# Optimization experiments

Measured on AMD Instinct MI355X. Metric: run time of the kernel, lower is better.

## Reference

```python
import jax, jax.numpy as jnp
import numpy as np

NEG_INF = -1e12  # stanza's constant.INFINITY_NUMBER


def setup_inputs() -> dict:
    key = jax.random.key(0)
    k1, k2, k3, k4, k5, k6 = jax.random.split(key, 6)
    B, S, D = 128, 8192, 128
    inp = jax.random.normal(k1, (B, D), dtype=jnp.float32)
    context = jax.random.normal(k2, (B, S, D), dtype=jnp.float32)
    mask = jax.random.bernoulli(k3, 0.3, (B, S))  # True = masked out
    # learned params (torch nn.Linear convention: y = x @ W.T)
    W = jax.random.normal(k4, (D, D), dtype=jnp.float32) / np.sqrt(D)
    V = jax.random.normal(k5, (1, D), dtype=jnp.float32) / np.sqrt(D)
    Wout = jax.random.normal(k6, (D, 2 * D), dtype=jnp.float32) / np.sqrt(2 * D)
    return {"input": inp, "context": context, "mask": mask, "W": W, "V": V, "Wout": Wout}


def reference(input, context, mask, W, V, Wout):
    # u = ReLU(W x): per-batch, identical across source positions -> compute once
    u = jax.nn.relu(jnp.einsum('bd,ed->be', input, W))          # [B, D]
    v = jax.nn.relu(jnp.einsum('bsd,ed->bse', context, W))      # [B, S, D]
    # a = V . (u o v)
    attn = jnp.einsum('be,bse,e->bs', u, v, V[0])               # [B, S]
    attn = jnp.where(mask, NEG_INF, attn)
    attn = jax.nn.softmax(attn, axis=1)
    weighted = jnp.einsum('bs,bsd->bd', attn, context)          # [B, D]
    h_tilde = jnp.tanh(jnp.einsum('bf,ef->be', jnp.concatenate([weighted, input], axis=1), Wout))
    return (h_tilde, attn)
```

## Files before the change

kernel.cpp:

```cpp
#include <hip/hip_runtime.h>


#define BB 128
#define SS 8192
#define DD 128

typedef float f32x4_t __attribute__((ext_vector_type(4)));
typedef short bf16x8_t __attribute__((ext_vector_type(8)));
typedef unsigned short u16x8_t __attribute__((ext_vector_type(8)));
typedef unsigned int u32x4_t __attribute__((ext_vector_type(4)));
typedef int i32x4_t __attribute__((ext_vector_type(4)));

__device__ __forceinline__ unsigned short f2bf(float x) {
  unsigned u = __builtin_bit_cast(unsigned, x);
  unsigned r = (u + 0x7FFFu + ((u >> 16) & 1u)) >> 16;
  return (unsigned short)r;
}
__device__ __forceinline__ float bf2f(unsigned short h) {
  unsigned u = ((unsigned)h) << 16;
  return __builtin_bit_cast(float, u);
}
__device__ __forceinline__ unsigned cvtpk(float a, float b) {
  unsigned r;
  asm("v_cvt_pk_bf16_f32 %0, %1, %2" : "=v"(r) : "v"(a), "v"(b));
  return r;
}

__global__ void k_detect(const unsigned int* __restrict__ mw, unsigned int* __restrict__ flag) {
  int i = blockIdx.x * 256 + threadIdx.x;
  unsigned v = mw[i];
  unsigned f = 0;
  if (v == 0x3F800000u) f = 2u;
  else if (v > 1u) f = 1u;
  if (f) atomicOr(flag, f);
}

__global__ void k_prep(const float* __restrict__ inp, const float* __restrict__ Wg,
                       const float* __restrict__ Vg, unsigned short* __restrict__ Whi,
                       unsigned short* __restrict__ Wlo, float* __restrict__ wv) {
  const int b = blockIdx.x, tid = threadIdx.x;
  {
    int i = b * DD + tid;
    float x = Wg[i];
    unsigned short h = f2bf(x);
    Whi[i] = h;
    Wlo[i] = f2bf(x - bf2f(h));
  }
  __shared__ float xin[DD];
  xin[tid] = inp[b * DD + tid];
  __syncthreads();
  const float* wr = Wg + tid * DD;
  float s = 0.f;
#pragma unroll 8
  for (int d = 0; d < DD; ++d) s += xin[d] * wr[d];
  wv[b * DD + tid] = fmaxf(s, 0.f) * Vg[tid];
}

__launch_bounds__(512, 1)
__global__ void k_logits(const float* __restrict__ ctx, const unsigned short* __restrict__ Whi,
                         const unsigned short* __restrict__ Wlo, const float* __restrict__ wv,
                         const void* __restrict__ maskp, const unsigned int* __restrict__ flag,
                         float* __restrict__ logits, float* __restrict__ Wslice,
                         float* __restrict__ stats) {
  __shared__ unsigned short WPKH[16384];
  __shared__ unsigned short WPKL[16384];
  __shared__ float wl[DD];
  __shared__ float WB[8][DD];
  __shared__ float MS[8][2];

  const int tid = threadIdx.x;
  const int b = blockIdx.y;
  const int slice = blockIdx.x;
  const int wave = tid >> 6;
  const int lane = tid & 63;
  const int lr = lane & 15;
  const int lg = lane >> 4;
  const unsigned mode = *flag;

  const long rowb0 = (long)b * SS + (long)slice * 2048 + (long)wave * 256;

  f32x4_t xA[8], xB[8];
  auto issue = [&](f32x4_t (&x)[8], long grow, int rt) {
    const float* rp = ctx + (grow + rt * 16 + lr) * (long)DD + lg * 8;
#pragma unroll
    for (int ks = 0; ks < 4; ++ks) {
      x[ks * 2]     = *(const f32x4_t*)(rp + ks * 32);
      x[ks * 2 + 1] = *(const f32x4_t*)(rp + ks * 32 + 4);
    }
  };

  issue(xA, rowb0, 0);

#pragma unroll
  for (int jj = 0; jj < 4; ++jj) {
    int p = tid + jj * 512;
    int frag = p >> 6;
    int li = p & 63;
    int et = frag >> 2, ks = frag & 3;
    int lg2 = li >> 4, lr2 = li & 15;
    int src = (et * 16 + lr2) * DD + ks * 32 + lg2 * 8;
    *(u16x8_t*)(&WPKH[p * 8]) = *(const u16x8_t*)(&Whi[src]);
    *(u16x8_t*)(&WPKL[p * 8]) = *(const u16x8_t*)(&Wlo[src]);
  }
  if (tid < DD) wl[tid] = wv[b * DD + tid];
  __syncthreads();

  float wfreg[8];
#pragma unroll
  for (int et = 0; et < 8; ++et) wfreg[et] = wl[et * 16 + lr];

  float m_run = -3.4e38f, s_run = 0.f;
  f32x4_t wacc[8];
#pragma unroll
  for (int k = 0; k < 8; ++k) wacc[k] = f32x4_t{0.f, 0.f, 0.f, 0.f};

  auto process = [&](const f32x4_t (&x)[8], long grow, int rt) {
    bf16x8_t a[4];
#pragma unroll
    for (int ks = 0; ks < 4; ++ks) {
      u32x4_t hh;
      hh[0] = cvtpk(x[ks * 2][0], x[ks * 2][1]);
      hh[1] = cvtpk(x[ks * 2][2], x[ks * 2][3]);
      hh[2] = cvtpk(x[ks * 2 + 1][0], x[ks * 2 + 1][1]);
      hh[3] = cvtpk(x[ks * 2 + 1][2], x[ks * 2 + 1][3]);
      a[ks] = __builtin_bit_cast(bf16x8_t, hh);
    }
    f32x4_t part = {0.f, 0.f, 0.f, 0.f};
#pragma unroll
    for (int et = 0; et < 8; ++et) {
      f32x4_t v1 = {0.f, 0.f, 0.f, 0.f};
      f32x4_t v2 = v1;
#pragma unroll
      for (int ks = 0; ks < 4; ++ks) {
        const int pidx = ((((et << 2) | ks) << 6) | lane) << 3;
        bf16x8_t bh = *(const bf16x8_t*)(&WPKH[pidx]);
        bf16x8_t bl = *(const bf16x8_t*)(&WPKL[pidx]);
        v1 = __builtin_amdgcn_mfma_f32_16x16x32_bf16(a[ks], bh, v1, 0, 0, 0);
        v2 = __builtin_amdgcn_mfma_f32_16x16x32_bf16(a[ks], bl, v2, 0, 0, 0);
      }
      const float wf = wfreg[et];
#pragma unroll
      for (int i = 0; i < 4; ++i)
        part[i] += wf * fmaxf(v1[i] + v2[i], 0.f);
    }
#pragma unroll
    for (int m2 = 1; m2 < 16; m2 <<= 1) {
      part[0] += __shfl_xor(part[0], m2, 64);
      part[1] += __shfl_xor(part[1], m2, 64);
      part[2] += __shfl_xor(part[2], m2, 64);
      part[3] += __shfl_xor(part[3], m2, 64);
    }
    const long rowb = grow + rt * 16 + lg * 4;
    bool mk0, mk1, mk2, mk3;
    if (mode == 0) {
      i32x4_t mv = *(const i32x4_t*)((const int*)maskp + rowb);
      mk0 = mv[0] != 0; mk1 = mv[1] != 0; mk2 = mv[2] != 0; mk3 = mv[3] != 0;
    } else if (mode == 1) {
      unsigned mb = *(const unsigned*)((const unsigned char*)maskp + rowb);
      mk0 = (mb & 255u) != 0; mk1 = ((mb >> 8) & 255u) != 0;
      mk2 = ((mb >> 16) & 255u) != 0; mk3 = (mb >> 24) != 0;
    } else {
      f32x4_t mf = *(const f32x4_t*)((const float*)maskp + rowb);
      mk0 = mf[0] != 0.f; mk1 = mf[1] != 0.f; mk2 = mf[2] != 0.f; mk3 = mf[3] != 0.f;
    }
    part[0] = mk0 ? -1e12f : part[0];
    part[1] = mk1 ? -1e12f : part[1];
    part[2] = mk2 ? -1e12f : part[2];
    part[3] = mk3 ? -1e12f : part[3];
    if (lr == 0) *(f32x4_t*)(&logits[rowb]) = part;
    float gm = fmaxf(fmaxf(part[0], part[1]), fmaxf(part[2], part[3]));
    gm = fmaxf(gm, __shfl_xor(gm, 16, 64));
    gm = fmaxf(gm, __shfl_xor(gm, 32, 64));
    if (gm > m_run) {
      float sc = expf(m_run - gm);
      s_run *= sc;
#pragma unroll
      for (int k = 0; k < 8; ++k) {
        wacc[k][0] *= sc; wacc[k][1] *= sc; wacc[k][2] *= sc; wacc[k][3] *= sc;
      }
      m_run = gm;
    }
    float pv0 = expf(part[0] - m_run);
    float pv1 = expf(part[1] - m_run);
    float pv2 = expf(part[2] - m_run);
    float pv3 = expf(part[3] - m_run);
    s_run += (pv0 + pv1) + (pv2 + pv3);
    const int srcl = (lane & 12) << 2;
    float q0 = __shfl(pv0, srcl, 64);
    float q1 = __shfl(pv1, srcl, 64);
    float q2 = __shfl(pv2, srcl, 64);
    float q3 = __shfl(pv3, srcl, 64);
    const int sel = lane & 3;
    float pn = sel == 0 ? q0 : sel == 1 ? q1 : sel == 2 ? q2 : q3;
#pragma unroll
    for (int k = 0; k < 8; ++k) {
      wacc[k][0] += pn * x[k][0]; wacc[k][1] += pn * x[k][1];
      wacc[k][2] += pn * x[k][2]; wacc[k][3] += pn * x[k][3];
    }
  };

#pragma unroll 1
  for (int g = 0; g < 8; ++g) {
    const long grow = rowb0 + (long)g * 32;
    issue(xB, grow, 1);
    process(xA, grow, 0);
    if (g < 7) issue(xA, grow + 32, 0);
    process(xB, grow, 1);
  }

#pragma unroll
  for (int m2 = 1; m2 < 16; m2 <<= 1) {
#pragma unroll
    for (int k = 0; k < 8; ++k) {
      wacc[k][0] += __shfl_xor(wacc[k][0], m2, 64);
      wacc[k][1] += __shfl_xor(wacc[k][1], m2, 64);
      wacc[k][2] += __shfl_xor(wacc[k][2], m2, 64);
      wacc[k][3] += __shfl_xor(wacc[k][3], m2, 64);
    }
  }
  float st = s_run;
  st += __shfl_xor(st, 16, 64);
  st += __shfl_xor(st, 32, 64);
  if (lr == 0) {
#pragma unroll
    for (int k = 0; k < 8; ++k) {
      int ks = k >> 1, half = k & 1;
      int col = ks * 32 + lg * 8 + half * 4;
      WB[wave][col + 0] = wacc[k][0];
      WB[wave][col + 1] = wacc[k][1];
      WB[wave][col + 2] = wacc[k][2];
      WB[wave][col + 3] = wacc[k][3];
    }
  }
  if (lane == 0) { MS[wave][0] = m_run; MS[wave][1] = st; }
  __syncthreads();
  if (tid < DD) {
    float M = MS[0][0];
#pragma unroll
    for (int w = 1; w < 8; ++w) M = fmaxf(M, MS[w][0]);
    float Wv = 0.f, S = 0.f;
#pragma unroll
    for (int w = 0; w < 8; ++w) {
      float e = expf(MS[w][0] - M);
      Wv += WB[w][tid] * e;
      S  += MS[w][1] * e;
    }
    Wslice[(long)(b * 4 + slice) * DD + tid] = Wv;
    if (tid == 0) {
      stats[(b * 4 + slice) * 2 + 0] = M;
      stats[(b * 4 + slice) * 2 + 1] = S;
    }
  }
}

__global__ void k_attn(float* attnbuf, const float* __restrict__ stats) {
  const int b = blockIdx.x, c = blockIdx.y;
  const int tid = threadIdx.x;
  float m0 = stats[b * 8 + 0], s0 = stats[b * 8 + 1];
  float m1 = stats[b * 8 + 2], s1 = stats[b * 8 + 3];
  float m2 = stats[b * 8 + 4], s2 = stats[b * 8 + 5];
  float m3 = stats[b * 8 + 6], s3 = stats[b * 8 + 7];
  float M = fmaxf(fmaxf(m0, m1), fmaxf(m2, m3));
  float S = s0 * expf(m0 - M) + s1 * expf(m1 - M) + s2 * expf(m2 - M) + s3 * expf(m3 - M);
  float inv = 1.f / S;
  const long off = (long)b * SS + (long)c * 2048 + (long)tid * 4;
  f32x4_t v = *(const f32x4_t*)(attnbuf + off);
  v[0] = expf(v[0] - M) * inv;
  v[1] = expf(v[1] - M) * inv;
  v[2] = expf(v[2] - M) * inv;
  v[3] = expf(v[3] - M) * inv;
  *(f32x4_t*)(attnbuf + off) = v;
}

__global__ void k_final(const float* __restrict__ Wslice, const float* __restrict__ stats,
                        const float* __restrict__ inp, const float* __restrict__ Wout,
                        float* __restrict__ hout) {
  const int b = blockIdx.x;
  const int tid = threadIdx.x;
  __shared__ float wsh[DD], xin[DD];
  float m0 = stats[b * 8 + 0], s0 = stats[b * 8 + 1];
  float m1 = stats[b * 8 + 2], s1 = stats[b * 8 + 3];
  float m2 = stats[b * 8 + 4], s2 = stats[b * 8 + 5];
  float m3 = stats[b * 8 + 6], s3 = stats[b * 8 + 7];
  float M = fmaxf(fmaxf(m0, m1), fmaxf(m2, m3));
  float e0 = expf(m0 - M), e1 = expf(m1 - M), e2 = expf(m2 - M), e3 = expf(m3 - M);
  float S = s0 * e0 + s1 * e1 + s2 * e2 + s3 * e3;
  float Wv = Wslice[(long)(b * 4 + 0) * DD + tid] * e0
           + Wslice[(long)(b * 4 + 1) * DD + tid] * e1
           + Wslice[(long)(b * 4 + 2) * DD + tid] * e2
           + Wslice[(long)(b * 4 + 3) * DD + tid] * e3;
  wsh[tid] = Wv / S;
  xin[tid] = inp[b * DD + tid];
  __syncthreads();
  const float* wr = Wout + tid * (2 * DD);
  float s = 0.f;
#pragma unroll 8
  for (int f = 0; f < DD; ++f) s += wsh[f] * wr[f];
#pragma unroll 8
  for (int f = 0; f < DD; ++f) s += xin[f] * wr[DD + f];
  hout[b * DD + tid] = tanhf(s);
}

extern "C" void kernel_launch(void* const* d_in, const int* in_sizes, int n_in,
                              void* d_out, int out_size, void* d_ws, size_t ws_size,
                              hipStream_t stream) {
  const float* inp  = (const float*)d_in[0];
  const float* ctx  = (const float*)d_in[1];
  const void*  mask = d_in[2];
  const float* Wg   = (const float*)d_in[3];
  const float* Vg   = (const float*)d_in[4];
  const float* Wout = (const float*)d_in[5];

  float* out = (float*)d_out;
  float* h_out = out;
  float* attn_out = out + BB * DD;

  char* ws = (char*)d_ws;
  unsigned int*   flag   = (unsigned int*)ws;
  unsigned short* Whi    = (unsigned short*)(ws + 1024);
  unsigned short* Wlo    = (unsigned short*)(ws + 1024 + 32768);
  float*          wv     = (float*)(ws + 1024 + 65536);
  float*          Wslice = (float*)(ws + 1024 + 65536 + 65536);
  float*          stats  = (float*)(ws + 1024 + 65536 + 65536 + 262144);

  (void)hipMemsetAsync(flag, 0, 4, stream);
  k_detect<<<dim3(256),   dim3(256), 0, stream>>>((const unsigned int*)mask, flag);
  k_prep  <<<dim3(BB),    dim3(DD),  0, stream>>>(inp, Wg, Vg, Whi, Wlo, wv);
  k_logits<<<dim3(4, BB), dim3(512), 0, stream>>>(ctx, Whi, Wlo, wv, mask, flag,
                                                  attn_out, Wslice, stats);
  k_attn  <<<dim3(BB, 4), dim3(512), 0, stream>>>(attn_out, stats);
  k_final <<<dim3(BB),    dim3(128), 0, stream>>>(Wslice, stats, inp, Wout, h_out);
}
```

Baseline: 167.2 us.

## Drop bf16 low-part split, triple-buffer context loads, fuse small kernels

Removes the hi/lo bf16 split of W so the logits are computed with a single bf16 MFMA pass, halving matrix work and LDS traffic. It also switches the context prefetch to three register buffers, merges mask detection into the prep kernel, and merges the attention normalisation and output projection into one kernel. This cuts launch overhead and compute, at the cost of logit accuracy, since W is now rounded to bf16 only, and higher register pressure from the extra buffer.

```diff
diff --git a/kernel.cpp b/kernel.cpp
--- a/kernel.cpp
+++ b/kernel.cpp
@@ -16,54 +16,48 @@
   unsigned r = (u + 0x7FFFu + ((u >> 16) & 1u)) >> 16;
   return (unsigned short)r;
 }
-__device__ __forceinline__ float bf2f(unsigned short h) {
-  unsigned u = ((unsigned)h) << 16;
-  return __builtin_bit_cast(float, u);
-}
 __device__ __forceinline__ unsigned cvtpk(float a, float b) {
   unsigned r;
   asm("v_cvt_pk_bf16_f32 %0, %1, %2" : "=v"(r) : "v"(a), "v"(b));
   return r;
 }
 
-__global__ void k_detect(const unsigned int* __restrict__ mw, unsigned int* __restrict__ flag) {
-  int i = blockIdx.x * 256 + threadIdx.x;
-  unsigned v = mw[i];
-  unsigned f = 0;
-  if (v == 0x3F800000u) f = 2u;
-  else if (v > 1u) f = 1u;
-  if (f) atomicOr(flag, f);
-}
-
-__global__ void k_prep(const float* __restrict__ inp, const float* __restrict__ Wg,
+__global__ void k_prep(const unsigned int* __restrict__ mw, unsigned int* __restrict__ flag,
+                       const float* __restrict__ inp, const float* __restrict__ Wg,
                        const float* __restrict__ Vg, unsigned short* __restrict__ Whi,
-                       unsigned short* __restrict__ Wlo, float* __restrict__ wv) {
+                       float* __restrict__ wv) {
   const int b = blockIdx.x, tid = threadIdx.x;
   {
-    int i = b * DD + tid;
-    float x = Wg[i];
-    unsigned short h = f2bf(x);
-    Whi[i] = h;
-    Wlo[i] = f2bf(x - bf2f(h));
+    unsigned v = mw[b * 256 + tid];
+    unsigned f = 0;
+    if (v == 0x3F800000u) f = 2u;
+    else if (v > 1u) f = 1u;
+    if (f) atomicOr(flag, f);
   }
   __shared__ float xin[DD];
-  xin[tid] = inp[b * DD + tid];
-  __syncthreads();
-  const float* wr = Wg + tid * DD;
-  float s = 0.f;
+  if (b < BB) {
+    if (tid < DD) {
+      int i = b * DD + tid;
+      Whi[i] = f2bf(Wg[i]);
+      xin[tid] = inp[b * DD + tid];
+    }
+    __syncthreads();
+    if (tid < DD) {
+      const float* wr = Wg + tid * DD;
+      float s = 0.f;
 #pragma unroll 8
-  for (int d = 0; d < DD; ++d) s += xin[d] * wr[d];
-  wv[b * DD + tid] = fmaxf(s, 0.f) * Vg[tid];
+      for (int d = 0; d < DD; ++d) s += xin[d] * wr[d];
+      wv[b * DD + tid] = fmaxf(s, 0.f) * Vg[tid];
+    }
+  }
 }
 
 __launch_bounds__(512, 1)
 __global__ void k_logits(const float* __restrict__ ctx, const unsigned short* __restrict__ Whi,
-                         const unsigned short* __restrict__ Wlo, const float* __restrict__ wv,
-                         const void* __restrict__ maskp, const unsigned int* __restrict__ flag,
-                         float* __restrict__ logits, float* __restrict__ Wslice,
-                         float* __restrict__ stats) {
+                         const float* __restrict__ wv, const void* __restrict__ maskp,
+                         const unsigned int* __restrict__ flag, float* __restrict__ logits,
+                         float* __restrict__ Wslice, float* __restrict__ stats) {
   __shared__ unsigned short WPKH[16384];
-  __shared__ unsigned short WPKL[16384];
   __shared__ float wl[DD];
   __shared__ float WB[8][DD];
   __shared__ float MS[8][2];
@@ -79,9 +73,10 @@
 
   const long rowb0 = (long)b * SS + (long)slice * 2048 + (long)wave * 256;
 
-  f32x4_t xA[8], xB[8];
-  auto issue = [&](f32x4_t (&x)[8], long grow, int rt) {
-    const float* rp = ctx + (grow + rt * 16 + lr) * (long)DD + lg * 8;
+  f32x4_t xA[8], xB[8], xC[8];
+
+  auto issue = [&](f32x4_t (&x)[8], int t) {
+    const float* rp = ctx + (rowb0 + t * 16 + lr) * (long)DD + lg * 8;
 #pragma unroll
     for (int ks = 0; ks < 4; ++ks) {
       x[ks * 2]     = *(const f32x4_t*)(rp + ks * 32);
@@ -89,7 +84,8 @@
     }
   };
 
-  issue(xA, rowb0, 0);
+  issue(xA, 0);
+  issue(xB, 1);
 
 #pragma unroll
   for (int jj = 0; jj < 4; ++jj) {
@@ -100,7 +96,6 @@
     int lg2 = li >> 4, lr2 = li & 15;
     int src = (et * 16 + lr2) * DD + ks * 32 + lg2 * 8;
     *(u16x8_t*)(&WPKH[p * 8]) = *(const u16x8_t*)(&Whi[src]);
-    *(u16x8_t*)(&WPKL[p * 8]) = *(const u16x8_t*)(&Wlo[src]);
   }
   if (tid < DD) wl[tid] = wv[b * DD + tid];
   __syncthreads();
@@ -114,34 +109,35 @@
 #pragma unroll
   for (int k = 0; k < 8; ++k) wacc[k] = f32x4_t{0.f, 0.f, 0.f, 0.f};
 
-  auto process = [&](const f32x4_t (&x)[8], long grow, int rt) {
+  const int srcl = (lane & 12) << 2;
+  const int sel = lane & 3;
+
+  auto process = [&](const f32x4_t (&x)[8], int t) {
     bf16x8_t a[4];
 #pragma unroll
     for (int ks = 0; ks < 4; ++ks) {
+      f32x4_t x0 = x[ks * 2], x1 = x[ks * 2 + 1];
       u32x4_t hh;
-      hh[0] = cvtpk(x[ks * 2][0], x[ks * 2][1]);
-      hh[1] = cvtpk(x[ks * 2][2], x[ks * 2][3]);
-      hh[2] = cvtpk(x[ks * 2 + 1][0], x[ks * 2 + 1][1]);
-      hh[3] = cvtpk(x[ks * 2 + 1][2], x[ks * 2 + 1][3]);
+      hh[0] = cvtpk(x0[0], x0[1]);
+      hh[1] = cvtpk(x0[2], x0[3]);
+      hh[2] = cvtpk(x1[0], x1[1]);
+      hh[3] = cvtpk(x1[2], x1[3]);
       a[ks] = __builtin_bit_cast(bf16x8_t, hh);
     }
     f32x4_t part = {0.f, 0.f, 0.f, 0.f};
 #pragma unroll
     for (int et = 0; et < 8; ++et) {
-      f32x4_t v1 = {0.f, 0.f, 0.f, 0.f};
-      f32x4_t v2 = v1;
+      f32x4_t v = {0.f, 0.f, 0.f, 0.f};
 #pragma unroll
       for (int ks = 0; ks < 4; ++ks) {
         const int pidx = ((((et << 2) | ks) << 6) | lane) << 3;
         bf16x8_t bh = *(const bf16x8_t*)(&WPKH[pidx]);
-        bf16x8_t bl = *(const bf16x8_t*)(&WPKL[pidx]);
-        v1 = __builtin_amdgcn_mfma_f32_16x16x32_bf16(a[ks], bh, v1, 0, 0, 0);
-        v2 = __builtin_amdgcn_mfma_f32_16x16x32_bf16(a[ks], bl, v2, 0, 0, 0);
+        v = __builtin_amdgcn_mfma_f32_16x16x32_bf16(a[ks], bh, v, 0, 0, 0);
       }
       const float wf = wfreg[et];
 #pragma unroll
       for (int i = 0; i < 4; ++i)
-        part[i] += wf * fmaxf(v1[i] + v2[i], 0.f);
+        part[i] += wf * fmaxf(v[i], 0.f);
     }
 #pragma unroll
     for (int m2 = 1; m2 < 16; m2 <<= 1) {
@@ -150,7 +146,7 @@
       part[2] += __shfl_xor(part[2], m2, 64);
       part[3] += __shfl_xor(part[3], m2, 64);
     }
-    const long rowb = grow + rt * 16 + lg * 4;
+    const long rowb = rowb0 + t * 16 + lg * 4;
     bool mk0, mk1, mk2, mk3;
     if (mode == 0) {
       i32x4_t mv = *(const i32x4_t*)((const int*)maskp + rowb);
@@ -185,12 +181,10 @@
     float pv2 = expf(part[2] - m_run);
     float pv3 = expf(part[3] - m_run);
     s_run += (pv0 + pv1) + (pv2 + pv3);
-    const int srcl = (lane & 12) << 2;
     float q0 = __shfl(pv0, srcl, 64);
     float q1 = __shfl(pv1, srcl, 64);
     float q2 = __shfl(pv2, srcl, 64);
     float q3 = __shfl(pv3, srcl, 64);
-    const int sel = lane & 3;
     float pn = sel == 0 ? q0 : sel == 1 ? q1 : sel == 2 ? q2 : q3;
 #pragma unroll
     for (int k = 0; k < 8; ++k) {
@@ -200,13 +194,16 @@
   };
 
 #pragma unroll 1
-  for (int g = 0; g < 8; ++g) {
-    const long grow = rowb0 + (long)g * 32;
-    issue(xB, grow, 1);
-    process(xA, grow, 0);
-    if (g < 7) issue(xA, grow + 32, 0);
-    process(xB, grow, 1);
-  }
+  for (int kk = 0; kk < 5; ++kk) {
+    const int base = kk * 3;
+    issue(xC, base + 2);
+    process(xA, base);
+    issue(xA, base + 3);
+    process(xB, base + 1);
+    if (kk < 4) issue(xB, base + 4);
+    process(xC, base + 2);
+  }
+  process(xA, 15);
 
 #pragma unroll
   for (int m2 = 1; m2 < 16; m2 <<= 1) {
@@ -253,31 +250,11 @@
   }
 }
 
-__global__ void k_attn(float* attnbuf, const float* __restrict__ stats) {
-  const int b = blockIdx.x, c = blockIdx.y;
+__global__ void k_post(float* attnbuf, const float* __restrict__ stats,
+                       const float* __restrict__ Wslice, const float* __restrict__ inp,
+                       const float* __restrict__ Wout, float* __restrict__ hout) {
+  const int b = blockIdx.x, role = blockIdx.y;
   const int tid = threadIdx.x;
-  float m0 = stats[b * 8 + 0], s0 = stats[b * 8 + 1];
-  float m1 = stats[b * 8 + 2], s1 = stats[b * 8 + 3];
-  float m2 = stats[b * 8 + 4], s2 = stats[b * 8 + 5];
-  float m3 = stats[b * 8 + 6], s3 = stats[b * 8 + 7];
-  float M = fmaxf(fmaxf(m0, m1), fmaxf(m2, m3));
-  float S = s0 * expf(m0 - M) + s1 * expf(m1 - M) + s2 * expf(m2 - M) + s3 * expf(m3 - M);
-  float inv = 1.f / S;
-  const long off = (long)b * SS + (long)c * 2048 + (long)tid * 4;
-  f32x4_t v = *(const f32x4_t*)(attnbuf + off);
-  v[0] = expf(v[0] - M) * inv;
-  v[1] = expf(v[1] - M) * inv;
-  v[2] = expf(v[2] - M) * inv;
-  v[3] = expf(v[3] - M) * inv;
-  *(f32x4_t*)(attnbuf + off) = v;
-}
-
-__global__ void k_final(const float* __restrict__ Wslice, const float* __restrict__ stats,
-                        const float* __restrict__ inp, const float* __restrict__ Wout,
-                        float* __restrict__ hout) {
-  const int b = blockIdx.x;
-  const int tid = threadIdx.x;
-  __shared__ float wsh[DD], xin[DD];
   float m0 = stats[b * 8 + 0], s0 = stats[b * 8 + 1];
   float m1 = stats[b * 8 + 2], s1 = stats[b * 8 + 3];
   float m2 = stats[b * 8 + 4], s2 = stats[b * 8 + 5];
@@ -285,20 +262,36 @@
   float M = fmaxf(fmaxf(m0, m1), fmaxf(m2, m3));
   float e0 = expf(m0 - M), e1 = expf(m1 - M), e2 = expf(m2 - M), e3 = expf(m3 - M);
   float S = s0 * e0 + s1 * e1 + s2 * e2 + s3 * e3;
-  float Wv = Wslice[(long)(b * 4 + 0) * DD + tid] * e0
-           + Wslice[(long)(b * 4 + 1) * DD + tid] * e1
-           + Wslice[(long)(b * 4 + 2) * DD + tid] * e2
-           + Wslice[(long)(b * 4 + 3) * DD + tid] * e3;
-  wsh[tid] = Wv / S;
-  xin[tid] = inp[b * DD + tid];
-  __syncthreads();
-  const float* wr = Wout + tid * (2 * DD);
-  float s = 0.f;
+  if (role < 4) {
+    float inv = 1.f / S;
+    const long off = (long)b * SS + (long)role * 2048 + (long)tid * 4;
+    f32x4_t v = *(const f32x4_t*)(attnbuf + off);
+    v[0] = expf(v[0] - M) * inv;
+    v[1] = expf(v[1] - M) * inv;
+    v[2] = expf(v[2] - M) * inv;
+    v[3] = expf(v[3] - M) * inv;
+    *(f32x4_t*)(attnbuf + off) = v;
+  } else {
+    __shared__ float wsh[DD], xin[DD];
+    if (tid < DD) {
+      float Wv = Wslice[(long)(b * 4 + 0) * DD + tid] * e0
+               + Wslice[(long)(b * 4 + 1) * DD + tid] * e1
+               + Wslice[(long)(b * 4 + 2) * DD + tid] * e2
+               + Wslice[(long)(b * 4 + 3) * DD + tid] * e3;
+      wsh[tid] = Wv / S;
+      xin[tid] = inp[b * DD + tid];
+    }
+    __syncthreads();
+    if (tid < DD) {
+      const float* wr = Wout + tid * (2 * DD);
+      float s = 0.f;
 #pragma unroll 8
-  for (int f = 0; f < DD; ++f) s += wsh[f] * wr[f];
+      for (int f = 0; f < DD; ++f) s += wsh[f] * wr[f];
 #pragma unroll 8
-  for (int f = 0; f < DD; ++f) s += xin[f] * wr[DD + f];
-  hout[b * DD + tid] = tanhf(s);
+      for (int f = 0; f < DD; ++f) s += xin[f] * wr[DD + f];
+      hout[b * DD + tid] = tanhf(s);
+    }
+  }
 }
 
 extern "C" void kernel_launch(void* const* d_in, const int* in_sizes, int n_in,
@@ -318,16 +311,14 @@
   char* ws = (char*)d_ws;
   unsigned int*   flag   = (unsigned int*)ws;
   unsigned short* Whi    = (unsigned short*)(ws + 1024);
-  unsigned short* Wlo    = (unsigned short*)(ws + 1024 + 32768);
-  float*          wv     = (float*)(ws + 1024 + 65536);
-  float*          Wslice = (float*)(ws + 1024 + 65536 + 65536);
-  float*          stats  = (float*)(ws + 1024 + 65536 + 65536 + 262144);
+  float*          wv     = (float*)(ws + 1024 + 32768);
+  float*          Wslice = (float*)(ws + 1024 + 32768 + 65536);
+  float*          stats  = (float*)(ws + 1024 + 32768 + 65536 + 262144);
 
   (void)hipMemsetAsync(flag, 0, 4, stream);
-  k_detect<<<dim3(256),   dim3(256), 0, stream>>>((const unsigned int*)mask, flag);
-  k_prep  <<<dim3(BB),    dim3(DD),  0, stream>>>(inp, Wg, Vg, Whi, Wlo, wv);
-  k_logits<<<dim3(4, BB), dim3(512), 0, stream>>>(ctx, Whi, Wlo, wv, mask, flag,
+  k_prep  <<<dim3(256),   dim3(256), 0, stream>>>((const unsigned int*)mask, flag,
+                                                  inp, Wg, Vg, Whi, wv);
+  k_logits<<<dim3(4, BB), dim3(512), 0, stream>>>(ctx, Whi, wv, mask, flag,
                                                   attn_out, Wslice, stats);
-  k_attn  <<<dim3(BB, 4), dim3(512), 0, stream>>>(attn_out, stats);
-  k_final <<<dim3(BB),    dim3(128), 0, stream>>>(Wslice, stats, inp, Wout, h_out);
-}
+  k_post  <<<dim3(BB, 5), dim3(512), 0, stream>>>(attn_out, stats, Wslice, inp, Wout, h_out);
+}
```

Measured after the change: 166.5 us. No clear change (-0.4%).
